# Kernel tuning notes

Hardware: AMD Instinct MI355X
Metric: run time of the kernel (lower is better)

Reference implementation:

```python
import jax, jax.numpy as jnp
import numpy as np


def gcn_conv(x, W, b, src, dst, n_nodes):
    """PyG GCNConv: linear transform, then symmetric-normalized sparse aggregation.
    src/dst already include self-loops. Messages flow src -> dst."""
    xw = x @ W  # [N, out]
    deg = jax.ops.segment_sum(jnp.ones_like(dst, dtype=xw.dtype), dst, num_segments=n_nodes)
    dinv = jnp.where(deg > 0, jax.lax.rsqrt(deg), 0.0)
    norm = dinv[src] * dinv[dst]  # [E]
    msg = xw[src] * norm[:, None]  # gather + scale
    out = jax.ops.segment_sum(msg, dst, num_segments=n_nodes)  # scatter-add
    return out + b


def setup_inputs() -> dict:
    key = jax.random.key(0)
    ks = jax.random.split(key, 5)
    N, E, C_in, C_out = 50000, 800000, 512, 128
    H = 2 * C_out
    x = jax.random.normal(ks[0], (N, C_in), dtype=jnp.float32)
    edge_index = jax.random.randint(ks[1], (2, E), 0, N, dtype=jnp.int64)
    def glorot(k, shape):
        lim = float(np.sqrt(6.0 / (shape[0] + shape[1])))
        return jax.random.uniform(k, shape, jnp.float32, -lim, lim)
    return {
        "x": x,
        "edge_index": edge_index,
        "W1": glorot(ks[2], (C_in, H)),
        "b1": jnp.zeros((H,), jnp.float32),
        "W_mu": glorot(ks[3], (H, C_out)),
        "b_mu": jnp.zeros((C_out,), jnp.float32),
        "W_ls": glorot(ks[4], (H, C_out)),
        "b_ls": jnp.zeros((C_out,), jnp.float32),
    }


def reference(x, edge_index, W1, b1, W_mu, b_mu, W_ls, b_ls):
    n_nodes = x.shape[0]
    # add self-loops (PyG GCNConv default add_self_loops=True)
    loops = jnp.arange(n_nodes, dtype=edge_index.dtype)
    src = jnp.concatenate([edge_index[0], loops])
    dst = jnp.concatenate([edge_index[1], loops])
    h = jax.nn.relu(gcn_conv(x, W1, b1, src, dst, n_nodes))
    mu = gcn_conv(h, W_mu, b_mu, src, dst, n_nodes)
    logstd = gcn_conv(h, W_ls, b_ls, src, dst, n_nodes)
    # stack so output is a single array [2, N, out_channels]
    return jnp.stack([mu, logstd])
```

## Files before the change

kernel.cpp:

```cpp
#include <hip/hip_runtime.h>

static inline int ceil_div(int a, int b) { return (a + b - 1) / b; }

typedef __attribute__((ext_vector_type(8))) __bf16 bf16x8;
typedef __attribute__((ext_vector_type(8))) unsigned short ushort8;
typedef __attribute__((ext_vector_type(4))) float f32x4;

__device__ __forceinline__ unsigned short f2bf(float f) {
    union { float f; unsigned u; } v; v.f = f;
    unsigned r = v.u + 0x7fffu + ((v.u >> 16) & 1u);
    return (unsigned short)(r >> 16);
}
__device__ __forceinline__ float blo(unsigned u) {
    union { unsigned u; float f; } x; x.u = u << 16; return x.f;
}
__device__ __forceinline__ float bhi(unsigned u) {
    union { unsigned u; float f; } x; x.u = u & 0xffff0000u; return x.f;
}

#define SWZ(r) ((((r) & 3) ^ (((r) >> 2) & 3)))

typedef __attribute__((address_space(3))) unsigned lds_uint;
typedef __attribute__((address_space(1))) const unsigned glb_uint;
__device__ __forceinline__ void gload_lds16(const unsigned short* g, unsigned short* l) {
    __builtin_amdgcn_global_load_lds((glb_uint*)g, (lds_uint*)l, 16, 0, 0);
}

__global__ __launch_bounds__(256) void k_prep(const int* __restrict__ dst, int E, int* __restrict__ cnt,
                                              const float* __restrict__ x, unsigned short* __restrict__ xb,
                                              long nx,
                                              const float* __restrict__ W1, const float* __restrict__ Wmu,
                                              const float* __restrict__ Wls, unsigned short* __restrict__ W1t,
                                              unsigned short* __restrict__ Wct, int K1, int H, int Cout,
                                              int nbCount, int nbX) {
    const int b = blockIdx.x;
    if (b < nbCount) {
        int e = b * 256 + threadIdx.x;
        if (e < E) atomicAdd(&cnt[dst[e]], 1);
    } else if (b < nbCount + nbX) {
        long i = (long)(b - nbCount) * 2048 + (long)threadIdx.x * 8;
        if (i < nx) {
            float4 a0 = *(const float4*)(x + i);
            float4 a1 = *(const float4*)(x + i + 4);
            ushort8 t;
            t[0] = f2bf(a0.x); t[1] = f2bf(a0.y); t[2] = f2bf(a0.z); t[3] = f2bf(a0.w);
            t[4] = f2bf(a1.x); t[5] = f2bf(a1.y); t[6] = f2bf(a1.z); t[7] = f2bf(a1.w);
            *(ushort8*)(xb + i) = t;
        }
    } else {
        int t = (b - nbCount - nbX) * 256 + threadIdx.x;
        int n1 = H * K1;
        int n2 = 2 * Cout * H;
        if (t < n1) {
            int c = t / K1, k = t - c * K1;
            W1t[t] = f2bf(W1[(size_t)k * H + c]);
        } else if (t < n1 + n2) {
            int u = t - n1;
            int c = u / H, k = u - c * H;
            float v = (c < Cout) ? Wmu[(size_t)k * Cout + c] : Wls[(size_t)k * Cout + (c - Cout)];
            Wct[u] = f2bf(v);
        }
    }
}

__global__ __launch_bounds__(256) void k_bsum(const int* __restrict__ cnt, int* __restrict__ bsum, int N) {
    __shared__ int ws[4];
    const int i = blockIdx.x * 256 + threadIdx.x;
    const int lane = threadIdx.x & 63, wave = threadIdx.x >> 6;
    int v = (i < N) ? cnt[i] + 1 : 0;
    for (int off = 32; off > 0; off >>= 1) v += __shfl_down(v, off);
    if (lane == 0) ws[wave] = v;
    __syncthreads();
    if (threadIdx.x == 0) bsum[blockIdx.x] = ws[0] + ws[1] + ws[2] + ws[3];
}

__global__ __launch_bounds__(256) void k_scan_bsum(const int* __restrict__ bsum, int* __restrict__ bbase,
                                                   int nb, int* __restrict__ row_ptr, int N) {
    __shared__ int ws[4];
    const int tid = threadIdx.x;
    const int lane = tid & 63, wave = tid >> 6;
    const int v = (tid < nb) ? bsum[tid] : 0;
    int x = v;
    for (int off = 1; off < 64; off <<= 1) {
        int t = __shfl_up(x, off);
        if (lane >= off) x += t;
    }
    if (lane == 63) ws[wave] = x;
    __syncthreads();
    if (tid == 0) {
        int r = 0;
        for (int i = 0; i < 4; ++i) { int t = ws[i]; ws[i] = r; r += t; }
        row_ptr[N] = r;
    }
    __syncthreads();
    if (tid < nb) bbase[tid] = ws[wave] + x - v;
}

__global__ __launch_bounds__(256) void k_scan_apply(const int* __restrict__ cnt, const int* __restrict__ bbase,
                                                    int* __restrict__ row_ptr, int* __restrict__ cursor,
                                                    float* __restrict__ dinv, int N) {
    __shared__ int ws[4];
    const int i = blockIdx.x * 256 + threadIdx.x;
    const int lane = threadIdx.x & 63, wave = threadIdx.x >> 6;
    const int c = (i < N) ? cnt[i] + 1 : 0;
    int x = c;
    for (int off = 1; off < 64; off <<= 1) {
        int t = __shfl_up(x, off);
        if (lane >= off) x += t;
    }
    if (lane == 63) ws[wave] = x;
    __syncthreads();
    if (threadIdx.x == 0) {
        int r = 0;
        for (int k = 0; k < 4; ++k) { int t = ws[k]; ws[k] = r; r += t; }
    }
    __syncthreads();
    if (i < N) {
        const int excl = bbase[blockIdx.x] + ws[wave] + x - c;
        row_ptr[i] = excl;
        cursor[i] = excl;
        dinv[i] = rsqrtf((float)c);
    }
}

__global__ void k_scatter(const int* __restrict__ src, const int* __restrict__ dst, int E, int N,
                          int* __restrict__ cursor, int* __restrict__ col) {
    int t = blockIdx.x * blockDim.x + threadIdx.x;
    if (t < E) {
        int p = atomicAdd(&cursor[dst[t]], 1);
        col[p] = src[t];
    } else if (t < E + N) {
        int n = t - E;
        int p = atomicAdd(&cursor[n], 1);
        col[p] = n;
    }
}

__device__ __forceinline__ void gemm_tile_core(const unsigned short* __restrict__ A,
                                               const unsigned short* __restrict__ B,
                                               unsigned short* __restrict__ As, unsigned short* __restrict__ Bs,
                                               int row0, int col0, int K,
                                               int wave, int lane, f32x4 (*acc)[4]) {
    const int quad = lane >> 4, l16 = lane & 15;
    const int rw = wave & 1, cw = wave >> 1;
    const int srow = wave * 32 + (lane >> 2);
    const int slot = lane & 3;
    for (int k0 = 0; k0 < K; k0 += 32) {
#pragma unroll
        for (int t = 0; t < 2; ++t) {
            const int lr = srow + t * 16;
            const int kc = (slot ^ SWZ(lr)) * 8;
            gload_lds16(A + (size_t)(row0 + lr) * K + k0 + kc, As + (wave * 32 + t * 16) * 32);
            gload_lds16(B + (size_t)(col0 + lr) * K + k0 + kc, Bs + (wave * 32 + t * 16) * 32);
        }
        __syncthreads();
        bf16x8 af[4], bf[4];
#pragma unroll
        for (int i = 0; i < 4; ++i) {
            const int lr = rw * 64 + i * 16 + l16;
            af[i] = *(const bf16x8*)&As[lr * 32 + ((quad ^ SWZ(lr))) * 8];
            const int lc = cw * 64 + i * 16 + l16;
            bf[i] = *(const bf16x8*)&Bs[lc * 32 + ((quad ^ SWZ(lc))) * 8];
        }
#pragma unroll
        for (int i = 0; i < 4; ++i)
#pragma unroll
            for (int j = 0; j < 4; ++j)
                acc[i][j] = __builtin_amdgcn_mfma_f32_16x16x32_bf16(af[i], bf[j], acc[i][j], 0, 0, 0);
        __syncthreads();
    }
}

__global__ __launch_bounds__(256) void k_gemm1(const unsigned short* __restrict__ xb,
                                               const unsigned short* __restrict__ W1t,
                                               unsigned short* __restrict__ y, int N, int K) {
    __shared__ __align__(16) unsigned short As[128 * 32];
    __shared__ __align__(16) unsigned short Bs[128 * 32];
    const int tid = threadIdx.x, wave = tid >> 6, lane = tid & 63;
    const int quad = lane >> 4, l16 = lane & 15;
    const int row0 = blockIdx.x * 128, col0 = blockIdx.y * 128;
    const int rw = wave & 1, cw = wave >> 1;
    f32x4 acc[4][4] = {};
    gemm_tile_core(xb, W1t, As, Bs, row0, col0, K, wave, lane, acc);
#pragma unroll
    for (int i = 0; i < 4; ++i) {
        const int grb = row0 + rw * 64 + i * 16 + quad * 4;
#pragma unroll
        for (int r = 0; r < 4; ++r) {
            const int row = grb + r;
            if (row < N) {
#pragma unroll
                for (int j = 0; j < 4; ++j)
                    y[(size_t)row * 256 + col0 + cw * 64 + j * 16 + l16] = f2bf(acc[i][j][r]);
            }
        }
    }
}

__global__ __launch_bounds__(256) void k_gemm2(const unsigned short* __restrict__ g,
                                               const unsigned short* __restrict__ Wct,
                                               const float* __restrict__ bmu, const float* __restrict__ bls,
                                               float* __restrict__ out, int N, int Cout) {
    __shared__ __align__(16) unsigned short As[128 * 32];
    __shared__ __align__(16) unsigned short Bs[128 * 32];
    const int K = 256;
    const int tid = threadIdx.x, wave = tid >> 6, lane = tid & 63;
    const int quad = lane >> 4, l16 = lane & 15;
    const int row0 = blockIdx.x * 128, col0 = blockIdx.y * 128;
    const int rw = wave & 1, cw = wave >> 1;
    f32x4 acc[4][4] = {};
    gemm_tile_core(g, Wct, As, Bs, row0, col0, K, wave, lane, acc);
#pragma unroll
    for (int j = 0; j < 4; ++j) {
        const int c = col0 + cw * 64 + j * 16 + l16;
        const bool is_mu = (c < Cout);
        const int ocl = is_mu ? c : (c - Cout);
        const float bv = is_mu ? bmu[ocl] : bls[ocl];
        const size_t obase = is_mu ? 0 : (size_t)N * Cout;
#pragma unroll
        for (int i = 0; i < 4; ++i) {
            const int grb = row0 + rw * 64 + i * 16 + quad * 4;
#pragma unroll
            for (int r = 0; r < 4; ++r) {
                const int row = grb + r;
                if (row < N) out[obase + (size_t)row * Cout + ocl] = acc[i][j][r] + bv;
            }
        }
    }
}

__global__ __launch_bounds__(256) void k_agg(const unsigned short* __restrict__ Yin,
                                             const int* __restrict__ row_ptr, const int* __restrict__ col,
                                             const float* __restrict__ dinv, const float* __restrict__ bias,
                                             unsigned short* __restrict__ Yout, int N, int relu_mode) {
    const int n = blockIdx.x * 4 + (threadIdx.x >> 6);
    if (n >= N) return;
    const int lane = threadIdx.x & 63;
    const int c = lane * 4;
    const int jb = row_ptr[n], je = row_ptr[n + 1];
    float ax0 = 0.f, ay0 = 0.f, az0 = 0.f, aw0 = 0.f;
    float ax1 = 0.f, ay1 = 0.f, az1 = 0.f, aw1 = 0.f;
    int j = jb;
    for (; j + 3 < je; j += 4) {
        const int s0 = col[j], s1 = col[j + 1], s2 = col[j + 2], s3 = col[j + 3];
        const float d0 = dinv[s0], d1 = dinv[s1], d2 = dinv[s2], d3 = dinv[s3];
        const uint2 v0 = *(const uint2*)(Yin + (size_t)s0 * 256 + c);
        const uint2 v1 = *(const uint2*)(Yin + (size_t)s1 * 256 + c);
        const uint2 v2 = *(const uint2*)(Yin + (size_t)s2 * 256 + c);
        const uint2 v3 = *(const uint2*)(Yin + (size_t)s3 * 256 + c);
        ax0 = fmaf(d0, blo(v0.x), fmaf(d1, blo(v1.x), ax0));
        ay0 = fmaf(d0, bhi(v0.x), fmaf(d1, bhi(v1.x), ay0));
        az0 = fmaf(d0, blo(v0.y), fmaf(d1, blo(v1.y), az0));
        aw0 = fmaf(d0, bhi(v0.y), fmaf(d1, bhi(v1.y), aw0));
        ax1 = fmaf(d2, blo(v2.x), fmaf(d3, blo(v3.x), ax1));
        ay1 = fmaf(d2, bhi(v2.x), fmaf(d3, bhi(v3.x), ay1));
        az1 = fmaf(d2, blo(v2.y), fmaf(d3, blo(v3.y), az1));
        aw1 = fmaf(d2, bhi(v2.y), fmaf(d3, bhi(v3.y), aw1));
    }
    for (; j < je; ++j) {
        const int s0 = col[j];
        const float d0 = dinv[s0];
        const uint2 v0 = *(const uint2*)(Yin + (size_t)s0 * 256 + c);
        ax0 = fmaf(d0, blo(v0.x), ax0);
        ay0 = fmaf(d0, bhi(v0.x), ay0);
        az0 = fmaf(d0, blo(v0.y), az0);
        aw0 = fmaf(d0, bhi(v0.y), aw0);
    }
    const float ax = ax0 + ax1, ay = ay0 + ay1, az = az0 + az1, aw = aw0 + aw1;
    const float dn = dinv[n];
    float ox, oy, oz, ow;
    if (relu_mode) {
        const float4 b = *(const float4*)&bias[c];
        ox = fmaxf(fmaf(dn, ax, b.x), 0.f);
        oy = fmaxf(fmaf(dn, ay, b.y), 0.f);
        oz = fmaxf(fmaf(dn, az, b.z), 0.f);
        ow = fmaxf(fmaf(dn, aw, b.w), 0.f);
    } else {
        ox = dn * ax; oy = dn * ay; oz = dn * az; ow = dn * aw;
    }
    uint2 o;
    o.x = (unsigned)f2bf(ox) | ((unsigned)f2bf(oy) << 16);
    o.y = (unsigned)f2bf(oz) | ((unsigned)f2bf(ow) << 16);
    *(uint2*)(Yout + (size_t)n * 256 + c) = o;
}


extern "C" void kernel_launch(void* const* d_in, const int* in_sizes, int n_in,
                              void* d_out, int out_size, void* d_ws, size_t ws_size,
                              hipStream_t stream) {
    const float* x   = (const float*)d_in[0];
    const int*   ei  = (const int*)d_in[1];
    const float* W1  = (const float*)d_in[2];
    const float* b1  = (const float*)d_in[3];
    const float* Wmu = (const float*)d_in[4];
    const float* bmu = (const float*)d_in[5];
    const float* Wls = (const float*)d_in[6];
    const float* bls = (const float*)d_in[7];

    const int H    = in_sizes[3];
    const int Cin  = in_sizes[2] / H;
    const int Cout = in_sizes[5];
    const int N    = in_sizes[0] / Cin;
    const int E    = in_sizes[1] / 2;
    const int* srcv = ei;
    const int* dstv = ei + E;

    char* w = (char*)d_ws;
    size_t off = 0;
    auto alloc = [&](size_t bytes) -> void* {
        void* p = w + off;
        off = (off + bytes + 255) & ~(size_t)255;
        return p;
    };
    const int nb = ceil_div(N, 256);
    int*            cnt     = (int*)alloc((size_t)N * 4);
    int*            cursor  = (int*)alloc((size_t)N * 4);
    int*            row_ptr = (int*)alloc((size_t)(N + 1) * 4);
    float*          dinv    = (float*)alloc((size_t)N * 4);
    int*            bsum    = (int*)alloc((size_t)nb * 4);
    int*            bbase   = (int*)alloc((size_t)nb * 4);
    int*            col     = (int*)alloc((size_t)(E + N) * 4);
    unsigned short* W1t     = (unsigned short*)alloc((size_t)H * Cin * 2);
    unsigned short* Wct     = (unsigned short*)alloc((size_t)2 * Cout * H * 2);
    unsigned short* xb      = (unsigned short*)alloc((size_t)N * Cin * 2);
    unsigned short* y       = (unsigned short*)alloc((size_t)N * H * 2);
    unsigned short* y2      = (unsigned short*)alloc((size_t)(N + 128) * H * 2);
    unsigned short* g       = y;
    (void)ws_size; (void)n_in; (void)out_size;

    hipMemsetAsync(cnt, 0, (size_t)N * 4, stream);

    const long nx = (long)N * Cin;
    const int nbCount = ceil_div(E, 256);
    const int nbX = (int)((nx + 2047) / 2048);
    const int nbW = ceil_div(H * Cin + 2 * Cout * H, 256);
    k_prep<<<nbCount + nbX + nbW, 256, 0, stream>>>(dstv, E, cnt, x, xb, nx, W1, Wmu, Wls, W1t, Wct,
                                                    Cin, H, Cout, nbCount, nbX);

    k_bsum<<<nb, 256, 0, stream>>>(cnt, bsum, N);
    k_scan_bsum<<<1, 256, 0, stream>>>(bsum, bbase, nb, row_ptr, N);
    k_scan_apply<<<nb, 256, 0, stream>>>(cnt, bbase, row_ptr, cursor, dinv, N);
    k_scatter<<<ceil_div(E + N, 256), 256, 0, stream>>>(srcv, dstv, E, N, cursor, col);

    dim3 g1(ceil_div(N, 128), 2);
    k_gemm1<<<g1, 256, 0, stream>>>(xb, W1t, y, N, Cin);

    k_agg<<<ceil_div(N, 4), 256, 0, stream>>>(y, row_ptr, col, dinv, b1, y2, N, 1);
    k_agg<<<ceil_div(N, 4), 256, 0, stream>>>(y2, row_ptr, col, dinv, nullptr, g, N, 0);

    dim3 g2(ceil_div(N, 128), 2);
    k_gemm2<<<g2, 256, 0, stream>>>(g, Wct, bmu, bls, (float*)d_out, N, Cout);
}
```

Measured before the change: 449.6 us.

## Replicate degree counters and scatter cursors to spread atomic contention

Degree counting and CSR scatter now use 16 replicated counter/cursor arrays, with each 256-edge block choosing a copy, so atomics from different blocks land on different addresses. The scan sums the copies per node and gives each copy its own sub-range, and the self-loop entry is written directly by the scan kernel instead of by atomics in the scatter. The x conversion blocks are also moved ahead of the counting blocks in the prep launch. The cost is a 16x larger memset and 16 strided reads per node in the scan kernels, and edge order within a row now depends on the copy layout.

```diff
diff --git a/kernel.cpp b/kernel.cpp
--- a/kernel.cpp
+++ b/kernel.cpp
@@ -5,6 +5,8 @@
 typedef __attribute__((ext_vector_type(8))) __bf16 bf16x8;
 typedef __attribute__((ext_vector_type(8))) unsigned short ushort8;
 typedef __attribute__((ext_vector_type(4))) float f32x4;
+
+#define NCOPY 16
 
 __device__ __forceinline__ unsigned short f2bf(float f) {
     union { float f; unsigned u; } v; v.f = f;
@@ -27,6 +29,7 @@
 }
 
 __global__ __launch_bounds__(256) void k_prep(const int* __restrict__ dst, int E, int* __restrict__ cnt,
+                                              int N,
                                               const float* __restrict__ x, unsigned short* __restrict__ xb,
                                               long nx,
                                               const float* __restrict__ W1, const float* __restrict__ Wmu,
@@ -34,11 +37,8 @@
                                               unsigned short* __restrict__ Wct, int K1, int H, int Cout,
                                               int nbCount, int nbX) {
     const int b = blockIdx.x;
-    if (b < nbCount) {
-        int e = b * 256 + threadIdx.x;
-        if (e < E) atomicAdd(&cnt[dst[e]], 1);
-    } else if (b < nbCount + nbX) {
-        long i = (long)(b - nbCount) * 2048 + (long)threadIdx.x * 8;
+    if (b < nbX) {
+        long i = (long)b * 2048 + (long)threadIdx.x * 8;
         if (i < nx) {
             float4 a0 = *(const float4*)(x + i);
             float4 a1 = *(const float4*)(x + i + 4);
@@ -47,8 +47,15 @@
             t[4] = f2bf(a1.x); t[5] = f2bf(a1.y); t[6] = f2bf(a1.z); t[7] = f2bf(a1.w);
             *(ushort8*)(xb + i) = t;
         }
+    } else if (b < nbX + nbCount) {
+        const int rb = b - nbX;
+        const int e = rb * 256 + threadIdx.x;
+        if (e < E) {
+            const int copy = rb & (NCOPY - 1);
+            atomicAdd(&cnt[(size_t)copy * N + dst[e]], 1);
+        }
     } else {
-        int t = (b - nbCount - nbX) * 256 + threadIdx.x;
+        int t = (b - nbX - nbCount) * 256 + threadIdx.x;
         int n1 = H * K1;
         int n2 = 2 * Cout * H;
         if (t < n1) {
@@ -63,11 +70,16 @@
     }
 }
 
-__global__ __launch_bounds__(256) void k_bsum(const int* __restrict__ cnt, int* __restrict__ bsum, int N) {
+__global__ __launch_bounds__(256) void k_bsum(const int* __restrict__ cnt, int N, int* __restrict__ bsum) {
     __shared__ int ws[4];
     const int i = blockIdx.x * 256 + threadIdx.x;
     const int lane = threadIdx.x & 63, wave = threadIdx.x >> 6;
-    int v = (i < N) ? cnt[i] + 1 : 0;
+    int v = 0;
+    if (i < N) {
+        v = 1;
+#pragma unroll
+        for (int c = 0; c < NCOPY; ++c) v += cnt[(size_t)c * N + i];
+    }
     for (int off = 32; off > 0; off >>= 1) v += __shfl_down(v, off);
     if (lane == 0) ws[wave] = v;
     __syncthreads();
@@ -96,14 +108,22 @@
     if (tid < nb) bbase[tid] = ws[wave] + x - v;
 }
 
-__global__ __launch_bounds__(256) void k_scan_apply(const int* __restrict__ cnt, const int* __restrict__ bbase,
+__global__ __launch_bounds__(256) void k_scan_apply(const int* __restrict__ cnt, int N,
+                                                    const int* __restrict__ bbase,
                                                     int* __restrict__ row_ptr, int* __restrict__ cursor,
-                                                    float* __restrict__ dinv, int N) {
+                                                    int* __restrict__ col,
+                                                    float* __restrict__ dinv) {
     __shared__ int ws[4];
     const int i = blockIdx.x * 256 + threadIdx.x;
     const int lane = threadIdx.x & 63, wave = threadIdx.x >> 6;
-    const int c = (i < N) ? cnt[i] + 1 : 0;
-    int x = c;
+    int cc[NCOPY];
+    int deg = 0;
+    if (i < N) {
+        deg = 1;
+#pragma unroll
+        for (int c = 0; c < NCOPY; ++c) { cc[c] = cnt[(size_t)c * N + i]; deg += cc[c]; }
+    }
+    int x = deg;
     for (int off = 1; off < 64; off <<= 1) {
         int t = __shfl_up(x, off);
         if (lane >= off) x += t;
@@ -116,23 +136,23 @@
     }
     __syncthreads();
     if (i < N) {
-        const int excl = bbase[blockIdx.x] + ws[wave] + x - c;
+        const int excl = bbase[blockIdx.x] + ws[wave] + x - deg;
         row_ptr[i] = excl;
-        cursor[i] = excl;
-        dinv[i] = rsqrtf((float)c);
+        dinv[i] = rsqrtf((float)deg);
+        int base = excl;
+#pragma unroll
+        for (int c = 0; c < NCOPY; ++c) { cursor[(size_t)c * N + i] = base; base += cc[c]; }
+        col[base] = i;
     }
 }
 
 __global__ void k_scatter(const int* __restrict__ src, const int* __restrict__ dst, int E, int N,
                           int* __restrict__ cursor, int* __restrict__ col) {
-    int t = blockIdx.x * blockDim.x + threadIdx.x;
+    const int t = blockIdx.x * blockDim.x + threadIdx.x;
     if (t < E) {
-        int p = atomicAdd(&cursor[dst[t]], 1);
+        const int copy = (t >> 8) & (NCOPY - 1);
+        const int p = atomicAdd(&cursor[(size_t)copy * N + dst[t]], 1);
         col[p] = src[t];
-    } else if (t < E + N) {
-        int n = t - E;
-        int p = atomicAdd(&cursor[n], 1);
-        col[p] = n;
     }
 }
 
@@ -313,8 +333,8 @@
         return p;
     };
     const int nb = ceil_div(N, 256);
-    int*            cnt     = (int*)alloc((size_t)N * 4);
-    int*            cursor  = (int*)alloc((size_t)N * 4);
+    int*            cnt     = (int*)alloc((size_t)NCOPY * N * 4);
+    int*            cursor  = (int*)alloc((size_t)NCOPY * N * 4);
     int*            row_ptr = (int*)alloc((size_t)(N + 1) * 4);
     float*          dinv    = (float*)alloc((size_t)N * 4);
     int*            bsum    = (int*)alloc((size_t)nb * 4);
@@ -328,19 +348,19 @@
     unsigned short* g       = y;
     (void)ws_size; (void)n_in; (void)out_size;
 
-    hipMemsetAsync(cnt, 0, (size_t)N * 4, stream);
+    hipMemsetAsync(cnt, 0, (size_t)NCOPY * N * 4, stream);
 
     const long nx = (long)N * Cin;
     const int nbCount = ceil_div(E, 256);
     const int nbX = (int)((nx + 2047) / 2048);
     const int nbW = ceil_div(H * Cin + 2 * Cout * H, 256);
-    k_prep<<<nbCount + nbX + nbW, 256, 0, stream>>>(dstv, E, cnt, x, xb, nx, W1, Wmu, Wls, W1t, Wct,
+    k_prep<<<nbX + nbCount + nbW, 256, 0, stream>>>(dstv, E, cnt, N, x, xb, nx, W1, Wmu, Wls, W1t, Wct,
                                                     Cin, H, Cout, nbCount, nbX);
 
-    k_bsum<<<nb, 256, 0, stream>>>(cnt, bsum, N);
+    k_bsum<<<nb, 256, 0, stream>>>(cnt, N, bsum);
     k_scan_bsum<<<1, 256, 0, stream>>>(bsum, bbase, nb, row_ptr, N);
-    k_scan_apply<<<nb, 256, 0, stream>>>(cnt, bbase, row_ptr, cursor, dinv, N);
-    k_scatter<<<ceil_div(E + N, 256), 256, 0, stream>>>(srcv, dstv, E, N, cursor, col);
+    k_scan_apply<<<nb, 256, 0, stream>>>(cnt, N, bbase, row_ptr, cursor, col, dinv);
+    k_scatter<<<ceil_div(E, 256), 256, 0, stream>>>(srcv, dstv, E, N, cursor, col);
 
     dim3 g1(ceil_div(N, 128), 2);
     k_gemm1<<<g1, 256, 0, stream>>>(xb, W1t, y, N, Cin);
```

New measurement: 434.6 us. 3.3% less time.
